# Performance work log

Measured on AMD Instinct MI355X. Metric: run time of the kernel, lower is better.

## Reference

```python
import jax, jax.numpy as jnp
import numpy as np

N_NODES = 50000
N_EDGES = 800000
N_GRAPHS = 64
NEG_SLOPE = 0.2  # PyG GATConv default leaky_relu slope
EPS = 1e-16      # PyG softmax denominator epsilon


def gat_conv(x, W, a_src, a_dst, bias, src, dst, n_nodes):
    """PyG GATConv (heads=1, concat=True, self-loops already appended).
    x: [N, F_in], W: [F_in, H*F], a_src/a_dst: [H, F], bias: [H*F]."""
    H, F = a_src.shape
    h = (x @ W).reshape(-1, H, F)                      # [N, H, F]
    alpha_src = jnp.einsum('nhf,hf->nh', h, a_src)     # [N, H]
    alpha_dst = jnp.einsum('nhf,hf->nh', h, a_dst)     # [N, H]
    e = jax.nn.leaky_relu(alpha_src[src] + alpha_dst[dst], NEG_SLOPE)  # [E, H]
    # segment softmax over incoming edges of each destination node
    e_max = jax.ops.segment_max(e, dst, num_segments=n_nodes)          # [N, H]
    e_exp = jnp.exp(e - e_max[dst])
    denom = jax.ops.segment_sum(e_exp, dst, num_segments=n_nodes)      # [N, H]
    alpha = e_exp / (denom[dst] + EPS)                                 # [E, H]
    msg = alpha[:, :, None] * h[src]                                   # [E, H, F]
    out = jax.ops.segment_sum(msg, dst, num_segments=n_nodes)          # [N, H, F]
    return out.reshape(-1, H * F) + bias


def global_mean_pool(x, batch, n_graphs):
    s = jax.ops.segment_sum(x, batch, num_segments=n_graphs)
    cnt = jax.ops.segment_sum(jnp.ones((x.shape[0],), x.dtype), batch, num_segments=n_graphs)
    return s / jnp.maximum(cnt, 1.0)[:, None]


def setup_inputs() -> dict:
    key = jax.random.key(0)
    ks = jax.random.split(key, 10)
    d_in, d_h, d_out, L, H = 128, 128, 10, 3, 1
    x = jax.random.normal(ks[0], (N_NODES, d_in), dtype=jnp.float32)
    edge_index = jax.random.randint(ks[1], (2, N_EDGES), 0, N_NODES, dtype=jnp.int32)
    edge_attr = jax.random.normal(ks[2], (N_EDGES, 4), dtype=jnp.float32)
    batch = jnp.sort(jax.random.randint(ks[3], (N_NODES,), 0, N_GRAPHS, dtype=jnp.int32))
    s0 = 1.0 / np.sqrt(d_in)
    sh = 1.0 / np.sqrt(d_h)
    return {
        'x': x,
        'edge_index': edge_index,
        'edge_attr': edge_attr,
        'batch': batch,
        'W0': jax.random.normal(ks[4], (d_in, d_h), dtype=jnp.float32) * s0,
        'b0': jnp.zeros((d_h,), jnp.float32),
        'Wc': jax.random.normal(ks[5], (L, d_h, H * d_h), dtype=jnp.float32) * sh,
        'att_src': jax.random.normal(ks[6], (L, H, d_h), dtype=jnp.float32) * sh,
        'att_dst': jax.random.normal(ks[7], (L, H, d_h), dtype=jnp.float32) * sh,
        'bc': jnp.zeros((L, H * d_h), jnp.float32),
        'W1': jax.random.normal(ks[8], (d_h, d_out), dtype=jnp.float32) * sh,
        'b1': jnp.zeros((d_out,), jnp.float32),
    }


def reference(x, edge_index, edge_attr, batch, W0, b0, Wc, att_src, att_dst, bc, W1, b1):
    n = x.shape[0]
    # GATConv default add_self_loops=True
    loops = jnp.arange(n, dtype=edge_index.dtype)
    src = jnp.concatenate([edge_index[0], loops])
    dst = jnp.concatenate([edge_index[1], loops])
    # dropout p=0 / eval mode -> identity
    h = jax.nn.relu(x @ W0 + b0)
    for i in range(Wc.shape[0]):
        h = jax.nn.relu(gat_conv(h, Wc[i], att_src[i], att_dst[i], bc[i], src, dst, n))
    pooled = global_mean_pool(h, batch, N_GRAPHS)   # [B, d_h]
    return pooled @ W1 + b1                          # [B, d_out]
```

## Files before the change

kernel.cpp:

```cpp
#include <hip/hip_runtime.h>
#include <hip/hip_bf16.h>
#include <hip/hip_fp16.h>
#include <hip/hip_fp8.h>

#define NN 50000
#define NE 800000
#define NG 64
#define DH 128

#define NPB 256
#define NBK ((NN + NPB - 1) / NPB)
#define EPB 4096
#define NPBLK ((NE + EPB - 1) / EPB)
#define CAPB 5120
#define GEMMB 782
#define CST 136
#define CSTB 136
#define SMEM_BYTES 18432

#if defined(__has_builtin)
# if __has_builtin(__builtin_amdgcn_cvt_pk_f32_fp8) && __has_builtin(__builtin_amdgcn_cvt_pk_fp8_f32)
#  define HW_FP8 1
# endif
#endif

typedef __bf16 bfx8 __attribute__((ext_vector_type(8)));
typedef float  f32x4 __attribute__((ext_vector_type(4)));

__device__ __forceinline__ ushort f2b(float f) {
    unsigned b = __float_as_uint(f);
    b += 0x7fff + ((b >> 16) & 1);
    return (ushort)(b >> 16);
}
__device__ __forceinline__ float b2f(ushort s) {
    return __uint_as_float((unsigned)s << 16);
}
__device__ __forceinline__ unsigned pk2(float a, float b) {
    return (unsigned)f2b(a) | ((unsigned)f2b(b) << 16);
}

__device__ __forceinline__ unsigned f2fp8(float v) {
    v = fminf(fmaxf(v, -448.f), 448.f);
#ifdef HW_FP8
    return (unsigned)__builtin_amdgcn_cvt_pk_fp8_f32(v, v, 0, false) & 0xFFu;
#else
    __hip_fp8_e4m3 t(v);
    return (unsigned)*(const unsigned char*)&t;
#endif
}
__device__ __forceinline__ void fp8x4_up(unsigned u, float* o) {
#ifdef HW_FP8
    auto lo = __builtin_amdgcn_cvt_pk_f32_fp8((int)u, false);
    auto hi = __builtin_amdgcn_cvt_pk_f32_fp8((int)u, true);
    o[0] = lo[0]; o[1] = lo[1]; o[2] = hi[0]; o[3] = hi[1];
#else
    #pragma unroll
    for (int k = 0; k < 4; ++k) {
        unsigned char c = (u >> (8 * k)) & 0xFF;
        o[k] = float(*(const __hip_fp8_e4m3*)&c);
    }
#endif
}

__launch_bounds__(256)
__global__ void k_partwt(const int* __restrict__ ei, int* __restrict__ gcur,
                         unsigned* __restrict__ tmp,
                         const float* __restrict__ W0, const float* __restrict__ Wc,
                         ushort* __restrict__ Wt) {
    int t = threadIdx.x;
    if (blockIdx.x >= NPBLK) {
        int i = (blockIdx.x - NPBLK) * 256 + t;
        int m = i >> 14;
        int r = i & 16383;
        int k = r >> 7, n = r & 127;
        const float* src = (m == 0) ? W0 : (Wc + (size_t)(m - 1) * DH * DH);
        Wt[(size_t)m * DH * DH + n * DH + k] = f2b(src[r]);
        return;
    }
    __shared__ int cnt[NBK], base[NBK], lcur[NBK];
    for (int i = t; i < NBK; i += 256) cnt[i] = 0;
    __syncthreads();
    int e0 = blockIdx.x * EPB;
    int dreg[16];
    #pragma unroll
    for (int j = 0; j < 16; ++j) {
        int e = e0 + j * 256 + t;
        dreg[j] = (e < NE) ? ei[NE + e] : -1;
        if (e < NE) atomicAdd(&cnt[dreg[j] >> 8], 1);
    }
    __syncthreads();
    for (int i = t; i < NBK; i += 256) {
        base[i] = cnt[i] ? atomicAdd(&gcur[i], cnt[i]) : 0;
        lcur[i] = 0;
    }
    __syncthreads();
    #pragma unroll
    for (int j = 0; j < 16; ++j) {
        int e = e0 + j * 256 + t;
        if (e < NE) {
            int d = dreg[j], s = ei[e];
            int b = d >> 8;
            int r = atomicAdd(&lcur[b], 1);
            tmp[(size_t)b * CAPB + base[b] + r] = ((unsigned)(d & 255) << 16) | (unsigned)s;
        }
    }
}

__launch_bounds__(256)
__global__ void k_bcount(const unsigned* __restrict__ tmp, const int* __restrict__ gcur,
                         int* __restrict__ deg, int* __restrict__ ploc,
                         int* __restrict__ bsizeP) {
    __shared__ int dcnt[NPB];
    int b = blockIdx.x, t = threadIdx.x;
    dcnt[t] = 0;
    __syncthreads();
    int ne = gcur[b];
    for (int e = t; e < ne; e += 256)
        atomicAdd(&dcnt[tmp[(size_t)b * CAPB + e] >> 16], 1);
    __syncthreads();
    int n = b * NPB + t;
    int d = (n < NN) ? dcnt[t] : 0;
    int p = (n < NN) ? ((d + 4) & ~3) : 0;
    int inc = p;
    #pragma unroll
    for (int off = 1; off < 64; off <<= 1) {
        int u = __shfl_up(inc, off);
        if ((t & 63) >= off) inc += u;
    }
    __shared__ int wsum[4];
    if ((t & 63) == 63) wsum[t >> 6] = inc;
    __syncthreads();
    int w = t >> 6, woff = 0;
    #pragma unroll
    for (int k = 0; k < 4; ++k) if (k < w) woff += wsum[k];
    int lofs = inc - p + woff;
    if (n < NN) { deg[n] = d; ploc[n] = lofs; }
    if (t == 255) bsizeP[b] = lofs + p;
}

template<bool AF32, bool DOTS, bool OUTFP8>
__device__ __forceinline__ void gemm_body(char* smem, int gblk,
        const void* __restrict__ Av, const ushort* __restrict__ Wt,
        const float* __restrict__ bias, void* __restrict__ C, int relu,
        const float* __restrict__ avs, const float* __restrict__ avd,
        float* __restrict__ asrc, float* __restrict__ adst) {
    int tid = threadIdx.x;
    int wid = (gblk * 256 + tid) >> 6;
    int lane = tid & 63;
    int row0 = wid * 16;
    if (row0 >= NN) return;
    int mrow = lane & 15;
    int quad = lane >> 4;
    int arow = row0 + mrow;

    f32x4 acc[8];
    #pragma unroll
    for (int t = 0; t < 8; ++t)
        #pragma unroll
        for (int r = 0; r < 4; ++r) acc[t][r] = 0.f;

    #pragma unroll
    for (int ks = 0; ks < 4; ++ks) {
        int k0 = ks * 32 + quad * 8;
        bfx8 a;
        if (AF32) {
            const float* ap = (const float*)Av + (size_t)arow * DH + k0;
            union { ushort s[8]; bfx8 v; } u;
            #pragma unroll
            for (int j = 0; j < 8; ++j) u.s[j] = f2b(ap[j]);
            a = u.v;
        } else {
            a = *(const bfx8*)((const ushort*)Av + (size_t)arow * DH + k0);
        }
        #pragma unroll
        for (int t = 0; t < 8; ++t) {
            bfx8 b = *(const bfx8*)(Wt + (size_t)(t * 16 + mrow) * DH + k0);
            acc[t] = __builtin_amdgcn_mfma_f32_16x16x32_bf16(a, b, acc[t], 0, 0, 0);
        }
    }

    if (OUTFP8) {
        uchar* my = (uchar*)smem + (tid >> 6) * 16 * CSTB;
        #pragma unroll
        for (int t = 0; t < 8; ++t) {
            int col = t * 16 + mrow;
            float bv = bias ? bias[col] : 0.f;
            #pragma unroll
            for (int r = 0; r < 4; ++r) {
                float v = acc[t][r] + bv;
                if (relu) v = fmaxf(v, 0.f);
                my[(quad * 4 + r) * CSTB + col] = (uchar)f2fp8(v);
            }
        }
        #pragma unroll
        for (int i = 0; i < 4; ++i) {
            int idx = i * 64 + lane;
            int row = idx >> 4;
            int c8 = idx & 15;
            uint2 u = *(const uint2*)(my + row * CSTB + c8 * 8);
            *(uint2*)((uchar*)C + (size_t)(row0 + row) * DH + c8 * 8) = u;
        }
    } else {
        ushort* my = (ushort*)smem + (tid >> 6) * 16 * CST;
        #pragma unroll
        for (int t = 0; t < 8; ++t) {
            int col = t * 16 + mrow;
            float bv = bias ? bias[col] : 0.f;
            #pragma unroll
            for (int r = 0; r < 4; ++r) {
                float v = acc[t][r] + bv;
                if (relu) v = fmaxf(v, 0.f);
                my[(quad * 4 + r) * CST + col] = f2b(v);
            }
        }
        #pragma unroll
        for (int i = 0; i < 4; ++i) {
            int idx = i * 64 + lane;
            int row = idx >> 4;
            int c16 = idx & 15;
            uint4 u = *(const uint4*)(my + row * CST + c16 * 8);
            *(uint4*)((ushort*)C + (size_t)(row0 + row) * DH + c16 * 8) = u;
        }
    }

    if (DOTS) {
        float av[8], dv[8];
        #pragma unroll
        for (int t = 0; t < 8; ++t) {
            av[t] = avs[t * 16 + mrow];
            dv[t] = avd[t * 16 + mrow];
        }
        int orow = row0 + quad * 4;
        #pragma unroll
        for (int r = 0; r < 4; ++r) {
            float ps = 0.f, pd = 0.f;
            #pragma unroll
            for (int t = 0; t < 8; ++t) {
                ps += acc[t][r] * av[t];
                pd += acc[t][r] * dv[t];
            }
            #pragma unroll
            for (int off = 1; off < 16; off <<= 1) {
                ps += __shfl_xor(ps, off);
                pd += __shfl_xor(pd, off);
            }
            if (mrow == 0) {
                asrc[orow + r] = ps;
                adst[orow + r] = pd;
            }
        }
    }
}

__launch_bounds__(256)
__global__ void k_buildgemm(const unsigned* __restrict__ tmp, const int* __restrict__ gcur,
                            const int* __restrict__ bsizeP, const int* __restrict__ ploc,
                            int* __restrict__ pstart, ushort* __restrict__ csr,
                            const float* __restrict__ x, const ushort* __restrict__ Wt,
                            const float* __restrict__ b0, ushort* __restrict__ hB) {
    __shared__ char smem[SMEM_BYTES];
    int t = threadIdx.x;
    if (blockIdx.x < GEMMB) {
        gemm_body<true, false, false>(smem, blockIdx.x, x, Wt, b0, hB, 1,
                                      nullptr, nullptr, nullptr, nullptr);
        return;
    }
    int b = blockIdx.x - GEMMB;
    ushort* buf = (ushort*)smem;
    int* lcur = (int*)(smem + 16384);
    int* sm   = (int*)(smem + 16384 + 1024);
    int v = (t < NBK) ? bsizeP[t] : 0;
    sm[t] = v;
    __syncthreads();
    for (int off = 1; off < 256; off <<= 1) {
        int u = (t >= off) ? sm[t - off] : 0;
        __syncthreads();
        sm[t] += u;
        __syncthreads();
    }
    int r0 = sm[b] - bsizeP[b];
    int S = bsizeP[b];
    int n0 = b * NPB, n1 = min(n0 + NPB, NN), nodes = n1 - n0;
    int ne = gcur[b];

    if (S <= 8192) {
        for (int i = t; i < (S >> 1); i += 256) ((unsigned*)buf)[i] = 0;
        __syncthreads();
        if (t < nodes) {
            int lp = ploc[n0 + t];
            pstart[n0 + t] = r0 + lp;
            lcur[t] = lp + 1;
            buf[lp] = (ushort)(n0 + t);
        }
        __syncthreads();
        for (int e = t; e < ne; e += 256) {
            unsigned u = tmp[(size_t)b * CAPB + e];
            int slot = atomicAdd(&lcur[u >> 16], 1);
            buf[slot] = (ushort)(u & 0xffffu);
        }
        __syncthreads();
        unsigned* dst = (unsigned*)(csr + r0);
        for (int i = t; i < (S >> 1); i += 256) dst[i] = ((unsigned*)buf)[i];
    } else {
        for (int i = t; i < S; i += 256) csr[r0 + i] = 0;
        __syncthreads();
        if (t < nodes) {
            int lp = ploc[n0 + t];
            pstart[n0 + t] = r0 + lp;
            lcur[t] = r0 + lp + 1;
            csr[r0 + lp] = (ushort)(n0 + t);
        }
        __syncthreads();
        for (int e = t; e < ne; e += 256) {
            unsigned u = tmp[(size_t)b * CAPB + e];
            int slot = atomicAdd(&lcur[u >> 16], 1);
            csr[slot] = (ushort)(u & 0xffffu);
        }
    }
}

__launch_bounds__(256)
__global__ void k_gemmdots(const ushort* __restrict__ hB, const ushort* __restrict__ Wt,
                           uchar* __restrict__ hA,
                           const float* __restrict__ avs, const float* __restrict__ avd,
                           float* __restrict__ asrc, float* __restrict__ adst) {
    __shared__ char smem[SMEM_BYTES];
    gemm_body<false, true, true>(smem, blockIdx.x, hB, Wt, nullptr, hA, 0,
                                 avs, avd, asrc, adst);
}

__launch_bounds__(256)
__global__ void k_aggr(const uchar* __restrict__ h8, const float* __restrict__ asrc,
                       const float* __restrict__ adst, const int* __restrict__ pstart,
                       const int* __restrict__ deg, const ushort* __restrict__ csr,
                       const float* __restrict__ bias, ushort* __restrict__ hout) {
    int wid = (blockIdx.x * blockDim.x + threadIdx.x) >> 6;
    int lane = threadIdx.x & 63;
    if (wid >= NN) return;
    int start = pstart[wid];
    int cnt = deg[wid] + 1;
    float ad = adst[wid];

    if (cnt <= 64) {
        int s = csr[start + lane];
        float e = -1e30f;
        if (lane < cnt) {
            float t = asrc[s] + ad;
            e = fmaxf(t, 0.f) + 0.2f * fminf(t, 0.f);
        }
        float m = e;
        #pragma unroll
        for (int off = 32; off; off >>= 1) m = fmaxf(m, __shfl_xor(m, off));
        float w = (lane < cnt) ? __expf(e - m) : 0.f;
        float dsum = w;
        #pragma unroll
        for (int off = 32; off; off >>= 1) dsum += __shfl_xor(dsum, off);

        int g = lane >> 4, fidx = lane & 15;
        float acc[8];
        #pragma unroll
        for (int k = 0; k < 8; ++k) acc[k] = 0.f;

        int steps = (cnt + 3) >> 2;
        const uint2* hp = (const uint2*)h8;
        int j = 0;
        for (; j + 3 < steps; j += 4) {
            int   e0 = j * 4 + g,      e1 = e0 + 4,  e2 = e0 + 8,  e3 = e0 + 12;
            float w0 = __shfl(w, e0),  w1 = __shfl(w, e1);
            float w2 = __shfl(w, e2),  w3 = __shfl(w, e3);
            int   s0 = __shfl(s, e0),  s1 = __shfl(s, e1);
            int   s2 = __shfl(s, e2),  s3 = __shfl(s, e3);
            uint2 u0 = hp[(size_t)s0 * 16 + fidx];
            uint2 u1 = hp[(size_t)s1 * 16 + fidx];
            uint2 u2 = hp[(size_t)s2 * 16 + fidx];
            uint2 u3 = hp[(size_t)s3 * 16 + fidx];
            float v[8];
            fp8x4_up(u0.x, v); fp8x4_up(u0.y, v + 4);
            #pragma unroll
            for (int k = 0; k < 8; ++k) acc[k] += w0 * v[k];
            fp8x4_up(u1.x, v); fp8x4_up(u1.y, v + 4);
            #pragma unroll
            for (int k = 0; k < 8; ++k) acc[k] += w1 * v[k];
            fp8x4_up(u2.x, v); fp8x4_up(u2.y, v + 4);
            #pragma unroll
            for (int k = 0; k < 8; ++k) acc[k] += w2 * v[k];
            fp8x4_up(u3.x, v); fp8x4_up(u3.y, v + 4);
            #pragma unroll
            for (int k = 0; k < 8; ++k) acc[k] += w3 * v[k];
        }
        for (; j < steps; ++j) {
            int e0 = j * 4 + g;
            float w0 = __shfl(w, e0);
            int   s0 = __shfl(s, e0);
            uint2 u0 = hp[(size_t)s0 * 16 + fidx];
            float v[8];
            fp8x4_up(u0.x, v); fp8x4_up(u0.y, v + 4);
            #pragma unroll
            for (int k = 0; k < 8; ++k) acc[k] += w0 * v[k];
        }
        #pragma unroll
        for (int k = 0; k < 8; ++k) {
            acc[k] += __shfl_xor(acc[k], 16);
            acc[k] += __shfl_xor(acc[k], 32);
        }
        if (g == 0) {
            float inv = 1.f / (dsum + 1e-16f);
            const float4* bp = (const float4*)bias;
            float4 b0 = bp[fidx * 2], b1 = bp[fidx * 2 + 1];
            uint4 o;
            o.x = pk2(fmaxf(acc[0] * inv + b0.x, 0.f), fmaxf(acc[1] * inv + b0.y, 0.f));
            o.y = pk2(fmaxf(acc[2] * inv + b0.z, 0.f), fmaxf(acc[3] * inv + b0.w, 0.f));
            o.z = pk2(fmaxf(acc[4] * inv + b1.x, 0.f), fmaxf(acc[5] * inv + b1.y, 0.f));
            o.w = pk2(fmaxf(acc[6] * inv + b1.z, 0.f), fmaxf(acc[7] * inv + b1.w, 0.f));
            ((uint4*)hout)[(size_t)wid * 16 + fidx] = o;
        }
        return;
    }

    float m = -1e30f;
    for (int i0 = start; i0 < start + cnt; i0 += 64) {
        int i = i0 + lane;
        float e = -1e30f;
        if (i < start + cnt) {
            int s = csr[i];
            float t = asrc[s] + ad;
            e = fmaxf(t, 0.f) + 0.2f * fminf(t, 0.f);
        }
        m = fmaxf(m, e);
    }
    #pragma unroll
    for (int off = 32; off; off >>= 1) m = fmaxf(m, __shfl_xor(m, off));

    float accx = 0.f, accy = 0.f, dsum = 0.f;
    for (int i0 = start; i0 < start + cnt; i0 += 64) {
        int i = i0 + lane;
        int s = 0; float w = 0.f;
        if (i < start + cnt) {
            s = csr[i];
            float t = asrc[s] + ad;
            float e = fmaxf(t, 0.f) + 0.2f * fminf(t, 0.f);
            w = __expf(e - m);
        }
        dsum += w;
        int cl = min(64, start + cnt - i0);
        for (int j = 0; j < cl; ++j) {
            int   sj = __shfl(s, j);
            float wj = __shfl(w, j);
            unsigned us = *(const ushort*)(h8 + (size_t)sj * DH + lane * 2);
            float v[4];
            fp8x4_up(us, v);
            accx += wj * v[0];
            accy += wj * v[1];
        }
    }
    #pragma unroll
    for (int off = 32; off; off >>= 1) dsum += __shfl_xor(dsum, off);

    float inv = 1.f / (dsum + 1e-16f);
    float ox = fmaxf(accx * inv + bias[lane * 2], 0.f);
    float oy = fmaxf(accy * inv + bias[lane * 2 + 1], 0.f);
    *(unsigned*)(hout + (size_t)wid * DH + lane * 2) = pk2(ox, oy);
}

__launch_bounds__(256)
__global__ void k_pool(const ushort* __restrict__ h, const int* __restrict__ batch,
                       float* __restrict__ gsum, int* __restrict__ gcnt) {
    int slot = threadIdx.x >> 7;
    int f = threadIdx.x & 127;
    int n0 = blockIdx.x * 64;
    int n1 = min(n0 + 64, NN);
    int first = n0 + slot;
    if (first >= n1) return;
    int g0 = batch[n0], g1 = batch[n1 - 1];
    if (g0 == g1) {
        float acc = 0.f;
        for (int nd = first; nd < n1; nd += 2)
            acc += b2f(h[(size_t)nd * DH + f]);
        atomicAdd(&gsum[g0 * DH + f], acc);
        if (f == 0 && slot == 0) atomicAdd(&gcnt[g0], n1 - n0);
        return;
    }
    float acc = 0.f; int run = 0;
    int gcur = batch[first];
    for (int nd = first; nd < n1; nd += 2) {
        int g = batch[nd];
        if (g != gcur) {
            atomicAdd(&gsum[gcur * DH + f], acc);
            if (f == 0) atomicAdd(&gcnt[gcur], run);
            acc = 0.f; run = 0; gcur = g;
        }
        acc += b2f(h[(size_t)nd * DH + f]);
        run += 1;
    }
    atomicAdd(&gsum[gcur * DH + f], acc);
    if (f == 0) atomicAdd(&gcnt[gcur], run);
}

__global__ void k_final(const float* __restrict__ gsum, const int* __restrict__ gcnt,
                        const float* __restrict__ W1, const float* __restrict__ b1,
                        float* __restrict__ out) {
    int t = threadIdx.x;
    if (t >= NG * 10) return;
    int g = t / 10, o = t % 10;
    float inv = 1.f / fmaxf((float)gcnt[g], 1.f);
    float acc = 0.f;
    for (int f = 0; f < DH; ++f) acc += gsum[g * DH + f] * W1[f * 10 + o];
    out[t] = acc * inv + b1[o];
}

extern "C" void kernel_launch(void* const* d_in, const int* in_sizes, int n_in,
                              void* d_out, int out_size, void* d_ws, size_t ws_size,
                              hipStream_t stream) {
    const float* x       = (const float*)d_in[0];
    const int*   ei      = (const int*)d_in[1];
    const int*   batch   = (const int*)d_in[3];
    const float* W0      = (const float*)d_in[4];
    const float* b0      = (const float*)d_in[5];
    const float* Wc      = (const float*)d_in[6];
    const float* att_src = (const float*)d_in[7];
    const float* att_dst = (const float*)d_in[8];
    const float* bc      = (const float*)d_in[9];
    const float* W1      = (const float*)d_in[10];
    const float* b1      = (const float*)d_in[11];
    float* out = (float*)d_out;

    char* ws = (char*)d_ws;
    size_t off = 0;
    auto alloc = [&](size_t bytes) {
        void* p = ws + off;
        off += (bytes + 255) & ~(size_t)255;
        return p;
    };
    uchar*    hA     = (uchar*)alloc((size_t)NN * DH);
    ushort*   hB     = (ushort*)alloc((size_t)NN * DH * 2);
    ushort*   Wt     = (ushort*)alloc((size_t)4 * DH * DH * 2);
    int*      pstart = (int*)alloc((size_t)NN * 4);
    ushort*   csr    = (ushort*)alloc((size_t)(NE + 4 * NN + 64) * 2);
    unsigned* tmp    = (unsigned*)alloc((size_t)NBK * CAPB * 4);
    float*    asrc   = (float*)alloc(NN * 4);
    float*    adst   = (float*)alloc(NN * 4);
    int*      deg    = (int*)alloc(NN * 4);
    int*      ploc   = (int*)alloc(NN * 4);
    int*      gcur   = (int*)alloc((NBK + 1) * 4);
    int*      bsizeP = (int*)alloc((NBK + 1) * 4);
    float*    gsum   = (float*)alloc(NG * DH * 4);
    int*      gcnt   = (int*)alloc(NG * 4);

    hipMemsetAsync(gcur, 0, (NBK + 1) * 4, stream);
    hipMemsetAsync(gsum, 0, NG * DH * 4 + 256, stream);

    k_partwt<<<NPBLK + 256, 256, 0, stream>>>(ei, gcur, tmp, W0, Wc, Wt);
    k_bcount<<<NBK, 256, 0, stream>>>(tmp, gcur, deg, ploc, bsizeP);
    k_buildgemm<<<GEMMB + NBK, 256, 0, stream>>>(tmp, gcur, bsizeP, ploc, pstart, csr,
                                                 x, Wt, b0, hB);

    for (int l = 0; l < 3; ++l) {
        k_gemmdots<<<GEMMB, 256, 0, stream>>>(hB, Wt + (size_t)(l + 1) * DH * DH, hA,
                                              att_src + l * DH, att_dst + l * DH,
                                              asrc, adst);
        k_aggr<<<(NN + 3) / 4, 256, 0, stream>>>(hA, asrc, adst, pstart, deg, csr,
                                                 bc + l * DH, hB);
    }

    k_pool<<<(NN + 63) / 64, 256, 0, stream>>>(hB, batch, gsum, gcnt);
    k_final<<<1, NG * 10, 0, stream>>>(gsum, gcnt, W1, b1, out);
}
```

Measured before the change: 325.7 us.

## Fuse whole GAT pipeline into one cooperative persistent kernel with grid syncs

Turns all stage kernels into device functions and runs them inside a single cooperative persistent kernel, using grid-wide barriers between stages. The CSR build step moves so that it overlaps with the layer-0 projection GEMM instead of the input GEMM. The aim is to remove launch overhead and the gaps between nine or more small kernels. In exchange it adds grid.sync costs and grid-stride loops over a grid capped by occupancy, and the gemm_body is no longer forced inline, which may raise register pressure. The original multi-launch path is kept as a fallback if the cooperative launch fails.

```diff
diff --git a/kernel.cpp b/kernel.cpp
--- a/kernel.cpp
+++ b/kernel.cpp
@@ -2,6 +2,9 @@
 #include <hip/hip_bf16.h>
 #include <hip/hip_fp16.h>
 #include <hip/hip_fp8.h>
+#include <hip/hip_cooperative_groups.h>
+
+namespace cg = cooperative_groups;
 
 #define NN 50000
 #define NE 800000
@@ -38,7 +41,6 @@
 __device__ __forceinline__ unsigned pk2(float a, float b) {
     return (unsigned)f2b(a) | ((unsigned)f2b(b) << 16);
 }
-
 __device__ __forceinline__ unsigned f2fp8(float v) {
     v = fminf(fmaxf(v, -448.f), 448.f);
 #ifdef HW_FP8
@@ -62,25 +64,16 @@
 #endif
 }
 
-__launch_bounds__(256)
-__global__ void k_partwt(const int* __restrict__ ei, int* __restrict__ gcur,
-                         unsigned* __restrict__ tmp,
-                         const float* __restrict__ W0, const float* __restrict__ Wc,
-                         ushort* __restrict__ Wt) {
+
+__device__ void part_body(char* smem, int vb, const int* __restrict__ ei,
+                          int* __restrict__ gcur, unsigned* __restrict__ tmp) {
+    int* cnt  = (int*)smem;
+    int* base = cnt + NBK;
+    int* lcur = base + NBK;
     int t = threadIdx.x;
-    if (blockIdx.x >= NPBLK) {
-        int i = (blockIdx.x - NPBLK) * 256 + t;
-        int m = i >> 14;
-        int r = i & 16383;
-        int k = r >> 7, n = r & 127;
-        const float* src = (m == 0) ? W0 : (Wc + (size_t)(m - 1) * DH * DH);
-        Wt[(size_t)m * DH * DH + n * DH + k] = f2b(src[r]);
-        return;
-    }
-    __shared__ int cnt[NBK], base[NBK], lcur[NBK];
     for (int i = t; i < NBK; i += 256) cnt[i] = 0;
     __syncthreads();
-    int e0 = blockIdx.x * EPB;
+    int e0 = vb * EPB;
     int dreg[16];
     #pragma unroll
     for (int j = 0; j < 16; ++j) {
@@ -106,12 +99,22 @@
     }
 }
 
-__launch_bounds__(256)
-__global__ void k_bcount(const unsigned* __restrict__ tmp, const int* __restrict__ gcur,
-                         int* __restrict__ deg, int* __restrict__ ploc,
-                         int* __restrict__ bsizeP) {
-    __shared__ int dcnt[NPB];
-    int b = blockIdx.x, t = threadIdx.x;
+__device__ void wt_body(int vb, const float* __restrict__ W0,
+                        const float* __restrict__ Wc, ushort* __restrict__ Wt) {
+    int i = vb * 256 + threadIdx.x;
+    int m = i >> 14;
+    int r = i & 16383;
+    int k = r >> 7, n = r & 127;
+    const float* src = (m == 0) ? W0 : (Wc + (size_t)(m - 1) * DH * DH);
+    Wt[(size_t)m * DH * DH + n * DH + k] = f2b(src[r]);
+}
+
+__device__ void bcount_body(char* smem, int b, const unsigned* __restrict__ tmp,
+                            const int* __restrict__ gcur, int* __restrict__ deg,
+                            int* __restrict__ ploc, int* __restrict__ bsizeP) {
+    int* dcnt = (int*)smem;
+    int* wsum = dcnt + NPB;
+    int t = threadIdx.x;
     dcnt[t] = 0;
     __syncthreads();
     int ne = gcur[b];
@@ -127,7 +130,6 @@
         int u = __shfl_up(inc, off);
         if ((t & 63) >= off) inc += u;
     }
-    __shared__ int wsum[4];
     if ((t & 63) == 63) wsum[t >> 6] = inc;
     __syncthreads();
     int w = t >> 6, woff = 0;
@@ -139,7 +141,7 @@
 }
 
 template<bool AF32, bool DOTS, bool OUTFP8>
-__device__ __forceinline__ void gemm_body(char* smem, int gblk,
+__device__ void gemm_body(char* smem, int gblk,
         const void* __restrict__ Av, const ushort* __restrict__ Wt,
         const float* __restrict__ bias, void* __restrict__ C, int relu,
         const float* __restrict__ avs, const float* __restrict__ avd,
@@ -252,23 +254,14 @@
     }
 }
 
-__launch_bounds__(256)
-__global__ void k_buildgemm(const unsigned* __restrict__ tmp, const int* __restrict__ gcur,
-                            const int* __restrict__ bsizeP, const int* __restrict__ ploc,
-                            int* __restrict__ pstart, ushort* __restrict__ csr,
-                            const float* __restrict__ x, const ushort* __restrict__ Wt,
-                            const float* __restrict__ b0, ushort* __restrict__ hB) {
-    __shared__ char smem[SMEM_BYTES];
-    int t = threadIdx.x;
-    if (blockIdx.x < GEMMB) {
-        gemm_body<true, false, false>(smem, blockIdx.x, x, Wt, b0, hB, 1,
-                                      nullptr, nullptr, nullptr, nullptr);
-        return;
-    }
-    int b = blockIdx.x - GEMMB;
+__device__ void build_body(char* smem, int b, const unsigned* __restrict__ tmp,
+                           const int* __restrict__ gcur, const int* __restrict__ bsizeP,
+                           const int* __restrict__ ploc, int* __restrict__ pstart,
+                           ushort* __restrict__ csr) {
     ushort* buf = (ushort*)smem;
     int* lcur = (int*)(smem + 16384);
     int* sm   = (int*)(smem + 16384 + 1024);
+    int t = threadIdx.x;
     int v = (t < NBK) ? bsizeP[t] : 0;
     sm[t] = v;
     __syncthreads();
@@ -319,24 +312,11 @@
     }
 }
 
-__launch_bounds__(256)
-__global__ void k_gemmdots(const ushort* __restrict__ hB, const ushort* __restrict__ Wt,
-                           uchar* __restrict__ hA,
-                           const float* __restrict__ avs, const float* __restrict__ avd,
-                           float* __restrict__ asrc, float* __restrict__ adst) {
-    __shared__ char smem[SMEM_BYTES];
-    gemm_body<false, true, true>(smem, blockIdx.x, hB, Wt, nullptr, hA, 0,
-                                 avs, avd, asrc, adst);
-}
-
-__launch_bounds__(256)
-__global__ void k_aggr(const uchar* __restrict__ h8, const float* __restrict__ asrc,
-                       const float* __restrict__ adst, const int* __restrict__ pstart,
-                       const int* __restrict__ deg, const ushort* __restrict__ csr,
-                       const float* __restrict__ bias, ushort* __restrict__ hout) {
-    int wid = (blockIdx.x * blockDim.x + threadIdx.x) >> 6;
-    int lane = threadIdx.x & 63;
-    if (wid >= NN) return;
+__device__ void aggr_wave(int wid, int lane, const uchar* __restrict__ h8,
+                          const float* __restrict__ asrc, const float* __restrict__ adst,
+                          const int* __restrict__ pstart, const int* __restrict__ deg,
+                          const ushort* __restrict__ csr, const float* __restrict__ bias,
+                          ushort* __restrict__ hout) {
     int start = pstart[wid];
     int cnt = deg[wid] + 1;
     float ad = adst[wid];
@@ -462,12 +442,12 @@
     *(unsigned*)(hout + (size_t)wid * DH + lane * 2) = pk2(ox, oy);
 }
 
-__launch_bounds__(256)
-__global__ void k_pool(const ushort* __restrict__ h, const int* __restrict__ batch,
-                       float* __restrict__ gsum, int* __restrict__ gcnt) {
+__device__ void pool_body(int vb, const ushort* __restrict__ h,
+                          const int* __restrict__ batch, float* __restrict__ gsum,
+                          int* __restrict__ gcnt) {
     int slot = threadIdx.x >> 7;
     int f = threadIdx.x & 127;
-    int n0 = blockIdx.x * 64;
+    int n0 = vb * 64;
     int n1 = min(n0 + 64, NN);
     int first = n0 + slot;
     if (first >= n1) return;
@@ -496,16 +476,119 @@
     if (f == 0) atomicAdd(&gcnt[gcur], run);
 }
 
-__global__ void k_final(const float* __restrict__ gsum, const int* __restrict__ gcnt,
-                        const float* __restrict__ W1, const float* __restrict__ b1,
-                        float* __restrict__ out) {
-    int t = threadIdx.x;
-    if (t >= NG * 10) return;
-    int g = t / 10, o = t % 10;
-    float inv = 1.f / fmaxf((float)gcnt[g], 1.f);
-    float acc = 0.f;
-    for (int f = 0; f < DH; ++f) acc += gsum[g * DH + f] * W1[f * 10 + o];
-    out[t] = acc * inv + b1[o];
+__device__ void final_body(const float* __restrict__ gsum, const int* __restrict__ gcnt,
+                           const float* __restrict__ W1, const float* __restrict__ b1,
+                           float* __restrict__ out) {
+    for (int t = threadIdx.x; t < NG * 10; t += 256) {
+        int g = t / 10, o = t % 10;
+        float inv = 1.f / fmaxf((float)gcnt[g], 1.f);
+        float acc = 0.f;
+        for (int f = 0; f < DH; ++f) acc += gsum[g * DH + f] * W1[f * 10 + o];
+        out[t] = acc * inv + b1[o];
+    }
+}
+
+__launch_bounds__(256)
+__global__ void k_mega(const int* ei, const float* x, const float* W0, const float* Wc,
+                       const float* b0, const float* att_src, const float* att_dst,
+                       const float* bc, const float* W1, const float* b1,
+                       const int* batch, float* out,
+                       uchar* hA, ushort* hB, ushort* Wt, int* pstart, ushort* csr,
+                       unsigned* tmp, float* asrc, float* adst, int* deg, int* ploc,
+                       int* gcur, int* bsizeP, float* gsum, int* gcnt) {
+    cg::grid_group grid = cg::this_grid();
+    __shared__ char smem[SMEM_BYTES];
+    int nb = gridDim.x;
+    int lane = threadIdx.x & 63;
+    int gw = (blockIdx.x * 256 + threadIdx.x) >> 6;
+    int wstride = nb * 4;
+
+    for (int vb = blockIdx.x; vb < NPBLK + 256; vb += nb) {
+        __syncthreads();
+        if (vb < NPBLK) part_body(smem, vb, ei, gcur, tmp);
+        else            wt_body(vb - NPBLK, W0, Wc, Wt);
+    }
+    grid.sync();
+
+    for (int vb = blockIdx.x; vb < NBK + GEMMB; vb += nb) {
+        __syncthreads();
+        if (vb < NBK) bcount_body(smem, vb, tmp, gcur, deg, ploc, bsizeP);
+        else gemm_body<true, false, false>(smem, vb - NBK, x, Wt, b0, hB, 1,
+                                           nullptr, nullptr, nullptr, nullptr);
+    }
+    grid.sync();
+
+    for (int l = 0; l < 3; ++l) {
+        int extra = (l == 0) ? NBK : 0;
+        const ushort* Wl = Wt + (size_t)(l + 1) * DH * DH;
+        for (int vb = blockIdx.x; vb < GEMMB + extra; vb += nb) {
+            __syncthreads();
+            if (vb < extra) build_body(smem, vb, tmp, gcur, bsizeP, ploc, pstart, csr);
+            else gemm_body<false, true, true>(smem, vb - extra, hB, Wl, nullptr, hA, 0,
+                                              att_src + l * DH, att_dst + l * DH,
+                                              asrc, adst);
+        }
+        grid.sync();
+        for (int wid = gw; wid < NN; wid += wstride)
+            aggr_wave(wid, lane, hA, asrc, adst, pstart, deg, csr, bc + l * DH, hB);
+        grid.sync();
+    }
+
+    for (int vb = blockIdx.x; vb < (NN + 63) / 64; vb += nb)
+        pool_body(vb, hB, batch, gsum, gcnt);
+    grid.sync();
+
+    if (blockIdx.x == 0) final_body(gsum, gcnt, W1, b1, out);
+}
+
+__launch_bounds__(256)
+__global__ void k_partwt(const int* ei, int* gcur, unsigned* tmp,
+                         const float* W0, const float* Wc, ushort* Wt) {
+    __shared__ char smem[SMEM_BYTES];
+    if (blockIdx.x < NPBLK) part_body(smem, blockIdx.x, ei, gcur, tmp);
+    else                    wt_body(blockIdx.x - NPBLK, W0, Wc, Wt);
+}
+__launch_bounds__(256)
+__global__ void k_bcount(const unsigned* tmp, const int* gcur, int* deg,
+                         int* ploc, int* bsizeP) {
+    __shared__ char smem[SMEM_BYTES];
+    bcount_body(smem, blockIdx.x, tmp, gcur, deg, ploc, bsizeP);
+}
+__launch_bounds__(256)
+__global__ void k_buildgemm(const unsigned* tmp, const int* gcur, const int* bsizeP,
+                            const int* ploc, int* pstart, ushort* csr,
+                            const float* x, const ushort* Wt, const float* b0,
+                            ushort* hB) {
+    __shared__ char smem[SMEM_BYTES];
+    if (blockIdx.x < GEMMB)
+        gemm_body<true, false, false>(smem, blockIdx.x, x, Wt, b0, hB, 1,
+                                      nullptr, nullptr, nullptr, nullptr);
+    else
+        build_body(smem, blockIdx.x - GEMMB, tmp, gcur, bsizeP, ploc, pstart, csr);
+}
+__launch_bounds__(256)
+__global__ void k_gemmdots(const ushort* hB, const ushort* Wt, uchar* hA,
+                           const float* avs, const float* avd,
+                           float* asrc, float* adst) {
+    __shared__ char smem[SMEM_BYTES];
+    gemm_body<false, true, true>(smem, blockIdx.x, hB, Wt, nullptr, hA, 0,
+                                 avs, avd, asrc, adst);
+}
+__launch_bounds__(256)
+__global__ void k_aggr(const uchar* h8, const float* asrc, const float* adst,
+                       const int* pstart, const int* deg, const ushort* csr,
+                       const float* bias, ushort* hout) {
+    int wid = (blockIdx.x * blockDim.x + threadIdx.x) >> 6;
+    if (wid >= NN) return;
+    aggr_wave(wid, threadIdx.x & 63, h8, asrc, adst, pstart, deg, csr, bias, hout);
+}
+__launch_bounds__(256)
+__global__ void k_pool(const ushort* h, const int* batch, float* gsum, int* gcnt) {
+    pool_body(blockIdx.x, h, batch, gsum, gcnt);
+}
+__global__ void k_final(const float* gsum, const int* gcnt, const float* W1,
+                        const float* b1, float* out) {
+    final_body(gsum, gcnt, W1, b1, out);
 }
 
 extern "C" void kernel_launch(void* const* d_in, const int* in_sizes, int n_in,
@@ -549,19 +632,37 @@
     hipMemsetAsync(gcur, 0, (NBK + 1) * 4, stream);
     hipMemsetAsync(gsum, 0, NG * DH * 4 + 256, stream);
 
-    k_partwt<<<NPBLK + 256, 256, 0, stream>>>(ei, gcur, tmp, W0, Wc, Wt);
-    k_bcount<<<NBK, 256, 0, stream>>>(tmp, gcur, deg, ploc, bsizeP);
-    k_buildgemm<<<GEMMB + NBK, 256, 0, stream>>>(tmp, gcur, bsizeP, ploc, pstart, csr,
-                                                 x, Wt, b0, hB);
-
-    for (int l = 0; l < 3; ++l) {
-        k_gemmdots<<<GEMMB, 256, 0, stream>>>(hB, Wt + (size_t)(l + 1) * DH * DH, hA,
-                                              att_src + l * DH, att_dst + l * DH,
-                                              asrc, adst);
-        k_aggr<<<(NN + 3) / 4, 256, 0, stream>>>(hA, asrc, adst, pstart, deg, csr,
-                                                 bc + l * DH, hB);
-    }
-
-    k_pool<<<(NN + 63) / 64, 256, 0, stream>>>(hB, batch, gsum, gcnt);
-    k_final<<<1, NG * 10, 0, stream>>>(gsum, gcnt, W1, b1, out);
-}
+    int maxPerCU = 0;
+    hipError_t occ = hipOccupancyMaxActiveBlocksPerMultiprocessor(
+        &maxPerCU, (const void*)k_mega, 256, 0);
+    bool coop_ok = (occ == hipSuccess) && (maxPerCU >= 1);
+    hipError_t lerr = hipErrorUnknown;
+    if (coop_ok) {
+        int grid = maxPerCU * 256;
+        if (grid > 2048) grid = 2048;
+        void* kargs[] = {
+            (void*)&ei, (void*)&x, (void*)&W0, (void*)&Wc, (void*)&b0,
+            (void*)&att_src, (void*)&att_dst, (void*)&bc, (void*)&W1, (void*)&b1,
+            (void*)&batch, (void*)&out, (void*)&hA, (void*)&hB, (void*)&Wt,
+            (void*)&pstart, (void*)&csr, (void*)&tmp, (void*)&asrc, (void*)&adst,
+            (void*)&deg, (void*)&ploc, (void*)&gcur, (void*)&bsizeP, (void*)&gsum,
+            (void*)&gcnt };
+        lerr = hipLaunchCooperativeKernel((const void*)k_mega, dim3(grid), dim3(256),
+                                          kargs, 0, stream);
+    }
+    if (lerr != hipSuccess) {
+        k_partwt<<<NPBLK + 256, 256, 0, stream>>>(ei, gcur, tmp, W0, Wc, Wt);
+        k_bcount<<<NBK, 256, 0, stream>>>(tmp, gcur, deg, ploc, bsizeP);
+        k_buildgemm<<<GEMMB + NBK, 256, 0, stream>>>(tmp, gcur, bsizeP, ploc, pstart,
+                                                     csr, x, Wt, b0, hB);
+        for (int l = 0; l < 3; ++l) {
+            k_gemmdots<<<GEMMB, 256, 0, stream>>>(hB, Wt + (size_t)(l + 1) * DH * DH,
+                                                  hA, att_src + l * DH,
+                                                  att_dst + l * DH, asrc, adst);
+            k_aggr<<<(NN + 3) / 4, 256, 0, stream>>>(hA, asrc, adst, pstart, deg, csr,
+                                                     bc + l * DH, hB);
+        }
+        k_pool<<<(NN + 63) / 64, 256, 0, stream>>>(hB, batch, gsum, gcnt);
+        k_final<<<1, NG * 10, 0, stream>>>(gsum, gcnt, W1, b1, out);
+    }
+}
```

Result: slower. 880.1 us (+170.2%).
